# Performance work log

Hardware: AMD Instinct MI355X
Metric: run time of the kernel (lower is better)

## Reference

```python
import jax, jax.numpy as jnp
import numpy as np

H, D = 4, 32            # heads, per-head dim
HD = H * D              # hidden_dim = output_dim = 128
ND, NG = 10000, 30000   # num disease / gene nodes
E_DG, E_GD, E_GG = 150000, 150000, 300000
L = 2                   # num HGTConv layers


def setup_inputs() -> dict:
    key = jax.random.key(0)
    ks = jax.random.split(key, 16)
    s = 0.05
    return {
        "x_d": jax.random.normal(ks[0], (ND, HD), jnp.float32),
        "x_g": jax.random.normal(ks[1], (NG, HD), jnp.float32),
        "src_dg": jax.random.randint(ks[2], (E_DG,), 0, ND),
        "dst_dg": jax.random.randint(ks[3], (E_DG,), 0, NG),
        "src_gd": jax.random.randint(ks[4], (E_GD,), 0, NG),
        "dst_gd": jax.random.randint(ks[5], (E_GD,), 0, ND),
        "src_gg": jax.random.randint(ks[6], (E_GG,), 0, NG),
        "dst_gg": jax.random.randint(ks[7], (E_GG,), 0, NG),
        # fused K/Q/V projection per node type, stacked over layers
        "Wkqv_d": jax.random.normal(ks[8], (L, HD, 3 * HD), jnp.float32) * s,
        "bkqv_d": jnp.zeros((L, 3 * HD), jnp.float32),
        "Wkqv_g": jax.random.normal(ks[9], (L, HD, 3 * HD), jnp.float32) * s,
        "bkqv_g": jnp.zeros((L, 3 * HD), jnp.float32),
        # output linear per node type
        "Wout_d": jax.random.normal(ks[10], (L, HD, HD), jnp.float32) * s,
        "bout_d": jnp.zeros((L, HD), jnp.float32),
        "Wout_g": jax.random.normal(ks[11], (L, HD, HD), jnp.float32) * s,
        "bout_g": jnp.zeros((L, HD), jnp.float32),
        # learnable skip gates per node type
        "skip_d": jnp.ones((L,), jnp.float32),
        "skip_g": jnp.ones((L,), jnp.float32),
        # per edge-type relation matrices (key, message) and priors, 3 edge types
        "arel": jax.random.normal(ks[12], (L, 3, H, D, D), jnp.float32) * s,
        "mrel": jax.random.normal(ks[13], (L, 3, H, D, D), jnp.float32) * s,
        "prel": jnp.ones((L, 3, H), jnp.float32),
    }


def _hgt_forward(x_d, x_g, src_dg, dst_dg, src_gd, dst_gd, src_gg, dst_gg,
                 Wkqv_d, bkqv_d, Wkqv_g, bkqv_g, Wout_d, bout_d, Wout_g, bout_g,
                 skip_d, skip_g, arel, mrel, prel):
    scale = 1.0 / (D ** 0.5)
    for l in range(L):
        def kqv(x, W, b):
            t = (x @ W + b).reshape(-1, 3, H, D)
            return t[:, 0], t[:, 1], t[:, 2]

        k_d, q_d, v_d = kqv(x_d, Wkqv_d[l], bkqv_d[l])
        k_g, q_g, v_g = kqv(x_g, Wkqv_g[l], bkqv_g[l])

        def edge_msgs(k_src, v_src, q_dst, src, dst, et):
            # gather src K/V, transform by per-edge-type relation matrices
            ke = jnp.einsum('ehd,hdf->ehf', k_src[src], arel[l, et])  # [E,H,D]
            ve = jnp.einsum('ehd,hdf->ehf', v_src[src], mrel[l, et])  # [E,H,D]
            a = jnp.sum(q_dst[dst] * ke, axis=-1) * prel[l, et] * scale  # [E,H]
            return a, ve

        a_dg, v_dg = edge_msgs(k_d, v_d, q_g, src_dg, dst_dg, 0)
        a_gd, v_gd = edge_msgs(k_g, v_g, q_d, src_gd, dst_gd, 1)
        a_gg, v_gg = edge_msgs(k_g, v_g, q_g, src_gg, dst_gg, 2)

        def aggregate(alphas, vals, dsts, n):
            # segment softmax over ALL incoming edges of a dst node (across edge types)
            a = jnp.concatenate(alphas, axis=0)
            v = jnp.concatenate(vals, axis=0)
            d = jnp.concatenate(dsts, axis=0)
            amax = jax.ops.segment_max(a, d, num_segments=n)
            ex = jnp.exp(a - amax[d])
            den = jax.ops.segment_sum(ex, d, num_segments=n)
            w = ex / den[d]
            out = jax.ops.segment_sum(w[:, :, None] * v, d, num_segments=n)
            return out.reshape(n, HD)

        agg_g = aggregate([a_dg, a_gg], [v_dg, v_gg], [dst_dg, dst_gg], NG)
        agg_d = aggregate([a_gd], [v_gd], [dst_gd], ND)

        def update(agg, x, Wout, bout, skip):
            o = jax.nn.gelu(agg) @ Wout + bout
            g = jax.nn.sigmoid(skip)
            return g * o + (1.0 - g) * x

        x_d = update(agg_d, x_d, Wout_d[l], bout_d[l], skip_d[l])
        x_g = update(agg_g, x_g, Wout_g[l], bout_g[l], skip_g[l])
    return x_d, x_g


def reference(x_d, x_g, src_dg, dst_dg, src_gd, dst_gd, src_gg, dst_gg,
              Wkqv_d, bkqv_d, Wkqv_g, bkqv_g, Wout_d, bout_d, Wout_g, bout_g,
              skip_d, skip_g, arel, mrel, prel):
    return _hgt_forward(x_d, x_g, src_dg, dst_dg, src_gd, dst_gd, src_gg, dst_gg,
                        Wkqv_d, bkqv_d, Wkqv_g, bkqv_g, Wout_d, bout_d, Wout_g, bout_g,
                        skip_d, skip_g, arel, mrel, prel)
```

## Files before the change

### kernel.cpp

```cpp
#include <hip/hip_runtime.h>
#include <hip/hip_bf16.h>

#define H 4
#define D 32
#define HD 128
#define ND 10000
#define NG 30000
#define E_DG 150000
#define E_GD 150000
#define E_GG 300000
#define NE (E_DG + E_GD + E_GG)
#define EG (E_DG + E_GG)
#define NLAYER 2
#define NBG 30
#define NBD 10
#define OCG 640
#define OCD 384
#define GOFF ((size_t)ND * OCD)
#define NSCAT 2344
#define NGEMM0 1250
#define XLSTRIDE 136

typedef _Float16 f16;
typedef __attribute__((ext_vector_type(2))) _Float16 f16x2;
typedef __attribute__((ext_vector_type(8))) _Float16 f16x8;
typedef __attribute__((ext_vector_type(8))) unsigned short u16x8;
typedef __attribute__((ext_vector_type(4))) float f32x4;

__device__ __forceinline__ float bu(unsigned short u) {
    return __uint_as_float(((unsigned)u) << 16);
}
__device__ __forceinline__ float ldraw(const void* p, size_t i, bool isf32) {
    return isf32 ? ((const float*)p)[i] : bu(((const unsigned short*)p)[i]);
}
__device__ __forceinline__ float gelu(float v) {
    const float c = 0.79788456080286536f * (v + 0.044715f * v * v * v);
    return 0.5f * v * (1.0f + tanhf(c));
}

__device__ __forceinline__ void combine_one(
    int idx, int GENE, bool isf32,
    const void* W, const void* bvec,
    const void* arel, const void* mrel, const void* prel,
    f16* __restrict__ Wp, float* __restrict__ bp) {
    const int OC = GENE ? OCG : OCD;
    const int l = idx / (OC * 128);
    const int rem = idx - l * OC * 128;
    const int col = rem >> 7;
    const int d = rem & 127;
    const int g = col >> 7;
    const int jj = col & 127;
    const int h = jj >> 5, f = jj & 31;
    const size_t wbase = (size_t)l * 128 * 384;
    const size_t bbase = (size_t)l * 384;
    float val, bv = 0.f;
    if (g == 0) {
        val = ldraw(W, wbase + d * 384 + 128 + jj, isf32);
        bv = ldraw(bvec, bbase + 128 + jj, isf32);
    } else {
        const int et = GENE ? ((g <= 2) ? 1 : 2) : 0;
        const bool isk = (g & 1);
        const void* mat = isk ? arel : mrel;
        const size_t mbase = (((size_t)(l * 3 + et) * H + h) << 10) + f;
        const int sb = isk ? 0 : 256;
        val = 0.f;
        for (int dd = 0; dd < 32; dd++)
            val += ldraw(W, wbase + d * 384 + sb + h * 32 + dd, isf32) *
                   ldraw(mat, mbase + dd * 32, isf32);
        if (d == 0)
            for (int dd = 0; dd < 32; dd++)
                bv += ldraw(bvec, bbase + sb + h * 32 + dd, isf32) *
                      ldraw(mat, mbase + dd * 32, isf32);
        if (isk) {
            const float sc = ldraw(prel, (size_t)(l * 3 + et) * H + h, isf32) *
                             (0.17677669529663689f * 1.4426950408889634f);
            val *= sc;
            bv *= sc;
        }
    }
    Wp[(size_t)l * 4 * OC * 32 + ((size_t)(d >> 5) * OC + col) * 32 + (d & 31)] = (f16)val;
    if (d == 0) bp[l * OC + col] = bv;
}

__global__ __launch_bounds__(256) void k_prep0(
    const void* x0,
    const void* wkqvd_r, const void* bkqvd_r,
    const void* wkqvg_r, const void* bkqvg_r,
    const void* arel_r, const void* mrel_r, const void* prel_r,
    const void* woutd_r, const void* woutg_r,
    const void* boutd_r, const void* boutg_r,
    const void* skipd_r, const void* skipg_r,
    f16* __restrict__ Wp_d, float* __restrict__ bp_d,
    f16* __restrict__ Wp_g, float* __restrict__ bp_g,
    f16* __restrict__ Wpod, f16* __restrict__ Wpog,
    float* __restrict__ boutc_d, float* __restrict__ boutc_g,
    float* __restrict__ gates, int* __restrict__ flag,
    int* __restrict__ cnt, int* __restrict__ ready) {
    const int tid = threadIdx.x;
    __shared__ int sbad;
    if (tid == 0) sbad = 0;
    __syncthreads();
    {
        const unsigned short* xs = (const unsigned short*)x0;
        int bad = 0;
        for (int i = tid; i < 1024; i += 256)
            if (!(fabsf(bu(xs[i])) < 1e6f)) bad = 1;
        if (bad) sbad = 1;
    }
    __syncthreads();
    const bool isf32 = (sbad != 0);

    const int b = blockIdx.x;
    if (b < 1280) {
        int idx = b * 256 + tid;
        const int nd = NLAYER * OCD * 128;
        const int ng = NLAYER * OCG * 128;
        const int np = 2 * NLAYER * 128 * 128;
        if (idx < nd) {
            combine_one(idx, 0, isf32, wkqvd_r, bkqvd_r, arel_r, mrel_r, prel_r, Wp_d, bp_d);
        } else if ((idx -= nd) < ng) {
            combine_one(idx, 1, isf32, wkqvg_r, bkqvg_r, arel_r, mrel_r, prel_r, Wp_g, bp_g);
        } else if ((idx -= ng) < np) {
            const int type = idx >= NLAYER * 128 * 128;
            int rem = idx - type * NLAYER * 128 * 128;
            const int l = rem / (128 * 128);
            rem -= l * 128 * 128;
            const int d = rem >> 7, col = rem & 127;
            const float w = ldraw(type ? woutg_r : woutd_r,
                                  (size_t)l * 128 * 128 + d * 128 + col, isf32);
            f16* out = (type ? Wpog : Wpod) +
                ((size_t)l * 4 + (d >> 5)) * 128 * 32 + col * 32 + (d & 31);
            *out = (f16)w;
        }
    } else if (b == 1280) {
        if (tid < NBG + NBD) ready[tid] = 0;
        if (tid == 0) {
            flag[0] = isf32 ? 1 : 0;
            gates[0] = 1.f / (1.f + expf(-ldraw(skipd_r, 0, isf32)));
            gates[1] = 1.f / (1.f + expf(-ldraw(skipg_r, 0, isf32)));
            gates[2] = 1.f / (1.f + expf(-ldraw(skipd_r, 1, isf32)));
            gates[3] = 1.f / (1.f + expf(-ldraw(skipg_r, 1, isf32)));
        }
        for (int i = tid; i < NLAYER * 128; i += 256) {
            boutc_d[i] = ldraw(boutd_r, i, isf32);
            boutc_g[i] = ldraw(boutg_r, i, isf32);
        }
    } else {
        const int base = (b - 1281) * 1000;
        for (int i = tid; i < 1000; i += 256) cnt[base + i] = 0;
    }
}

__global__ __launch_bounds__(256) void k_hist(
    const int* __restrict__ dst_dg, const int* __restrict__ dst_gg,
    const int* __restrict__ dst_gd,
    int* __restrict__ cnt_g, int* __restrict__ cnt_d) {
    const int i = blockIdx.x * 256 + threadIdx.x;
    if (i < E_DG) atomicAdd(cnt_g + dst_dg[i], 1);
    else if (i < EG) atomicAdd(cnt_g + dst_gg[i - E_DG], 1);
    else if (i < NE) atomicAdd(cnt_d + dst_gd[i - EG], 1);
}

__global__ __launch_bounds__(256) void k_scan(
    const int* __restrict__ cnt_g, const int* __restrict__ cnt_d,
    int* __restrict__ ready,
    int* __restrict__ rp_g, int* __restrict__ cur_g,
    int* __restrict__ rp_d, int* __restrict__ cur_d) {
    const int b = blockIdx.x;
    const int tid = threadIdx.x;
    const bool isg = (b < NBG);
    const int* cnt = isg ? cnt_g : cnt_d;
    int* rp = isg ? rp_g : rp_d;
    int* cur = isg ? cur_g : cur_d;
    const int n = isg ? NG : ND;
    const int lb = isg ? b : (b - NBG);
    const int i0 = lb * 1024 + tid * 4;
    int v[4];
    int t = 0;
#pragma unroll
    for (int j = 0; j < 4; j++) {
        v[j] = (i0 + j < n) ? cnt[i0 + j] : 0;
        t += v[j];
    }
    __shared__ int sdata[256];
    __shared__ int red2[256];
    __shared__ int s_off;
    sdata[tid] = t;
    __syncthreads();
    for (int d = 1; d < 256; d <<= 1) {
        const int u = (tid >= d) ? sdata[tid - d] : 0;
        __syncthreads();
        sdata[tid] += u;
        __syncthreads();
    }
    const int total = sdata[255];
    if (tid == 0) atomicExch(&ready[b], total + 1);
    const int p0 = isg ? 0 : NBG;
    const int npred = b - p0;
    int part = 0;
    for (int i = tid; i < npred; i += 256) {
        int vv;
        do { vv = atomicAdd(&ready[p0 + i], 0); } while (vv == 0);
        part += vv - 1;
    }
    red2[tid] = part;
    __syncthreads();
    for (int d = 128; d > 0; d >>= 1) {
        if (tid < d) red2[tid] += red2[tid + d];
        __syncthreads();
    }
    if (tid == 0) s_off = red2[0];
    __syncthreads();
    int run = s_off + sdata[tid] - t;
#pragma unroll
    for (int j = 0; j < 4; j++) {
        if (i0 + j < n) {
            cur[i0 + j] = run;
            run += v[j];
            rp[i0 + j + 1] = run;
        }
    }
    if (tid == 0 && lb == 0) rp[0] = 0;
}

__global__ __launch_bounds__(256) void k_scatter_gemm0(
    const int* __restrict__ src_dg, const int* __restrict__ dst_dg,
    const int* __restrict__ src_gg, const int* __restrict__ dst_gg,
    const int* __restrict__ src_gd, const int* __restrict__ dst_gd,
    int* __restrict__ cur_g, int* __restrict__ cur_d,
    int* __restrict__ edges_g, int* __restrict__ edges_d,
    const void* xd_r, const void* xg_r, const int* __restrict__ flag,
    const f16* __restrict__ Wpd, const float* __restrict__ bpd,
    const f16* __restrict__ Wpg, const float* __restrict__ bpg,
    f16* __restrict__ tab) {
    __shared__ f16 xls[32 * XLSTRIDE];
    if (blockIdx.x < NSCAT) {
        const int i = blockIdx.x * 256 + threadIdx.x;
        if (i < E_DG) {
            const int pos = atomicAdd(cur_g + dst_dg[i], 1);
            edges_g[pos] = src_dg[i] * OCD + 128;
        } else if (i < EG) {
            const int j = i - E_DG;
            const int pos = atomicAdd(cur_g + dst_gg[j], 1);
            edges_g[pos] = (int)GOFF + src_gg[j] * OCG + 384;
        } else if (i < NE) {
            const int j = i - EG;
            const int pos = atomicAdd(cur_d + dst_gd[j], 1);
            edges_d[pos] = (int)GOFF + src_gd[j] * OCG + 128;
        }
        return;
    }
    const bool isf32 = (*flag != 0);
    const int tid = threadIdx.x;
    const int mt0 = (blockIdx.x - NSCAT) * 2;
    for (int i = tid; i < 1024; i += 256) {
        const int row = i >> 5;
        const int c4 = (i & 31) * 4;
        const int gnode = mt0 * 16 + row;
        const bool gene = (gnode >= ND);
        const void* xr = gene ? xg_r : xd_r;
        const size_t base = (size_t)(gene ? gnode - ND : gnode) * 128 + c4;
        float4 v;
        if (isf32) {
            v = *(const float4*)((const float*)xr + base);
        } else {
            const ushort4 u = *(const ushort4*)((const unsigned short*)xr + base);
            v = make_float4(bu(u.x), bu(u.y), bu(u.z), bu(u.w));
        }
        f16* dst = xls + row * XLSTRIDE + c4;
        dst[0] = (f16)v.x; dst[1] = (f16)v.y; dst[2] = (f16)v.z; dst[3] = (f16)v.w;
    }
    __syncthreads();

    const int wv = tid >> 6, lane = tid & 63;
    const int r = lane & 15, q4 = lane >> 4;
    const int n0 = (mt0 * 16 >= ND) ? 10 : 6;
    const int n1 = ((mt0 + 1) * 16 >= ND) ? 10 : 6;
    for (int it = wv; it < n0 + n1; it += 4) {
        const int mtl = (it < n0) ? 0 : 1;
        const int ntl = (it < n0) ? it : (it - n0);
        const int node0 = (mt0 + mtl) * 16;
        const bool gene = (node0 >= ND);
        const int OC = gene ? OCG : OCD;
        const f16* Wp = gene ? Wpg : Wpd;
        const float* bias = gene ? bpg : bpd;
        f16* out = gene ? (tab + GOFF) : tab;
        const int trow0 = node0 - (gene ? ND : 0);
        const int col0 = ntl << 6;
        f32x4 acc0 = {0.f, 0.f, 0.f, 0.f};
        f32x4 acc1 = acc0, acc2 = acc0, acc3 = acc0;
#pragma unroll
        for (int kb = 0; kb < 4; kb++) {
            const f16x8 a = *(const f16x8*)(xls + (mtl * 16 + r) * XLSTRIDE + kb * 32 + q4 * 8);
            const f16* wb = Wp + ((size_t)kb * OC + col0 + r) * 32 + q4 * 8;
            const f16x8 b0 = *(const f16x8*)(wb);
            const f16x8 b1 = *(const f16x8*)(wb + 512);
            const f16x8 b2 = *(const f16x8*)(wb + 1024);
            const f16x8 b3 = *(const f16x8*)(wb + 1536);
            acc0 = __builtin_amdgcn_mfma_f32_16x16x32_f16(a, b0, acc0, 0, 0, 0);
            acc1 = __builtin_amdgcn_mfma_f32_16x16x32_f16(a, b1, acc1, 0, 0, 0);
            acc2 = __builtin_amdgcn_mfma_f32_16x16x32_f16(a, b2, acc2, 0, 0, 0);
            acc3 = __builtin_amdgcn_mfma_f32_16x16x32_f16(a, b3, acc3, 0, 0, 0);
        }
        const f32x4 accs[4] = {acc0, acc1, acc2, acc3};
#pragma unroll
        for (int t = 0; t < 4; t++) {
            const int col = col0 + t * 16 + r;
            const float bb = bias[col];
#pragma unroll
            for (int reg = 0; reg < 4; reg++)
                out[(size_t)(trow0 + q4 * 4 + reg) * OC + col] = (f16)(accs[t][reg] + bb);
        }
    }
}

__global__ __launch_bounds__(256) void k_agg(
    const int* __restrict__ rp_g, const int* __restrict__ edges_g,
    const int* __restrict__ rp_d, const int* __restrict__ edges_d,
    const f16* __restrict__ tab, f16* __restrict__ gagg) {
    const int wid = blockIdx.x * 4 + (threadIdx.x >> 6);
    const int lane = threadIdx.x & 63;
    const int slot = lane >> 4, sub = lane & 15;

    int node, row;
    const int *rp, *edges;
    size_t qoff;
    if (wid < NG) {
        node = wid; rp = rp_g; edges = edges_g;
        qoff = GOFF + (size_t)node * OCG;
        row = ND + node;
    } else {
        node = wid - NG; rp = rp_d; edges = edges_d;
        qoff = (size_t)node * OCD;
        row = node;
    }

    union U { f16x8 v; f16x2 p[4]; };
    U q;
    q.v = *(const f16x8*)(tab + qoff + sub * 8);

    float s = 0.f;
    float acc[8];
#pragma unroll
    for (int i = 0; i < 8; i++) acc[i] = 0.f;

    const int r0 = rp[node], r1 = rp[node + 1];
    int e = r0 + slot;

    auto kvload = [&](int rec, U& k, U& v) {
        const f16* p = tab + (size_t)rec + sub * 8;
        k.v = *(const f16x8*)p;
        v.v = *(const f16x8*)(p + 128);
    };

    int recA0 = (e < r1) ? edges[e] : 0;
    int recB0 = (e + 4 < r1) ? edges[e + 4] : 0;
    U kA0, vA0, kB0, vB0;
    kvload(recA0, kA0, vA0);
    kvload(recB0, kB0, vB0);
    int recA1 = (e + 8 < r1) ? edges[e + 8] : 0;
    int recB1 = (e + 12 < r1) ? edges[e + 12] : 0;

    while (e < r1) {
        const int recA2 = (e + 16 < r1) ? edges[e + 16] : 0;
        const int recB2 = (e + 20 < r1) ? edges[e + 20] : 0;
        U kA1, vA1, kB1, vB1;
        kvload(recA1, kA1, vA1);
        kvload(recB1, kB1, vB1);

        float pA = __builtin_amdgcn_fdot2(q.p[0], kA0.p[0], 0.f, false);
        float pB = __builtin_amdgcn_fdot2(q.p[0], kB0.p[0], 0.f, false);
        pA = __builtin_amdgcn_fdot2(q.p[1], kA0.p[1], pA, false);
        pB = __builtin_amdgcn_fdot2(q.p[1], kB0.p[1], pB, false);
        pA = __builtin_amdgcn_fdot2(q.p[2], kA0.p[2], pA, false);
        pB = __builtin_amdgcn_fdot2(q.p[2], kB0.p[2], pB, false);
        pA = __builtin_amdgcn_fdot2(q.p[3], kA0.p[3], pA, false);
        pB = __builtin_amdgcn_fdot2(q.p[3], kB0.p[3], pB, false);
        pA += __shfl_xor(pA, 1);
        pB += __shfl_xor(pB, 1);
        pA += __shfl_xor(pA, 2);
        pB += __shfl_xor(pB, 2);
        const float eaA = exp2f(pA);
        const float eaB = (e + 4 < r1) ? exp2f(pB) : 0.f;
        s += eaA + eaB;
#pragma unroll
        for (int i = 0; i < 8; i++)
            acc[i] = fmaf(eaB, (float)vB0.v[i], fmaf(eaA, (float)vA0.v[i], acc[i]));
        recA0 = recA1; recB0 = recB1; recA1 = recA2; recB1 = recB2;
        kA0 = kA1; vA0 = vA1; kB0 = kB1; vB0 = vB1;
        e += 8;
    }

#pragma unroll
    for (int mask = 16; mask <= 32; mask <<= 1) {
        s += __shfl_xor(s, mask);
#pragma unroll
        for (int i = 0; i < 8; i++) acc[i] += __shfl_xor(acc[i], mask);
    }

    const float inv = (s > 0.f) ? (1.f / s) : 0.f;
    if (slot == 0) {
        f16x8 o;
#pragma unroll
        for (int i = 0; i < 8; i++) o[i] = (f16)gelu(acc[i] * inv);
        *(f16x8*)(gagg + (size_t)row * HD + sub * 8) = o;
    }
}

__global__ __launch_bounds__(256) void k_updgemm(
    const f16* __restrict__ gagg,
    const f16* __restrict__ Wpod0, const f16* __restrict__ Wpog0,
    const float* __restrict__ boutc_d0, const float* __restrict__ boutc_g0,
    const float* __restrict__ gates,
    const void* xd_r, const void* xg_r, const int* __restrict__ flag,
    f16* __restrict__ xball,
    const f16* __restrict__ Wpd1, const float* __restrict__ bpd1,
    const f16* __restrict__ Wpg1, const float* __restrict__ bpg1,
    f16* __restrict__ tab) {
    __shared__ f16 xls[32 * XLSTRIDE];
    const bool isf32 = (*flag != 0);
    const int tid = threadIdx.x;
    const int wv = tid >> 6, lane = tid & 63;
    const int r = lane & 15, q4 = lane >> 4;

    {
        const int mtl = wv >> 1, nt = wv & 1;
        const int mtile = blockIdx.x * 2 + mtl;
        const int node0 = mtile * 16;
        const bool gene = (node0 >= ND);
        const f16* Wp = gene ? Wpog0 : Wpod0;
        const float* bias = gene ? boutc_g0 : boutc_d0;
        const float g = gates[gene ? 1 : 0];
        const int col0 = nt << 6;
        f32x4 acc0 = {0.f, 0.f, 0.f, 0.f};
        f32x4 acc1 = acc0, acc2 = acc0, acc3 = acc0;
#pragma unroll
        for (int kb = 0; kb < 4; kb++) {
            const f16x8 a = *(const f16x8*)(gagg + (size_t)(node0 + r) * 128 + kb * 32 + q4 * 8);
            const f16* wb = Wp + ((size_t)kb * 128 + col0 + r) * 32 + q4 * 8;
            const f16x8 b0 = *(const f16x8*)(wb);
            const f16x8 b1 = *(const f16x8*)(wb + 512);
            const f16x8 b2 = *(const f16x8*)(wb + 1024);
            const f16x8 b3 = *(const f16x8*)(wb + 1536);
            acc0 = __builtin_amdgcn_mfma_f32_16x16x32_f16(a, b0, acc0, 0, 0, 0);
            acc1 = __builtin_amdgcn_mfma_f32_16x16x32_f16(a, b1, acc1, 0, 0, 0);
            acc2 = __builtin_amdgcn_mfma_f32_16x16x32_f16(a, b2, acc2, 0, 0, 0);
            acc3 = __builtin_amdgcn_mfma_f32_16x16x32_f16(a, b3, acc3, 0, 0, 0);
        }
        const f32x4 accs[4] = {acc0, acc1, acc2, acc3};
        const void* xr = gene ? xg_r : xd_r;
        const int lrow0 = node0 - (gene ? ND : 0);
#pragma unroll
        for (int t = 0; t < 4; t++) {
            const int col = col0 + t * 16 + r;
            const float bb = bias[col];
#pragma unroll
            for (int reg = 0; reg < 4; reg++) {
                const int rr = q4 * 4 + reg;
                const float xo = ldraw(xr, (size_t)(lrow0 + rr) * 128 + col, isf32);
                const float xn = g * (accs[t][reg] + bb) + (1.f - g) * xo;
                xls[(mtl * 16 + rr) * XLSTRIDE + col] = (f16)xn;
                xball[(size_t)(node0 + rr) * 128 + col] = (f16)xn;
            }
        }
    }
    __syncthreads();

    const int mt0 = blockIdx.x * 2;
    const int n0 = ((mt0 * 16) >= ND) ? 10 : 6;
    const int n1 = (((mt0 + 1) * 16) >= ND) ? 10 : 6;
    for (int it = wv; it < n0 + n1; it += 4) {
        const int mtl = (it < n0) ? 0 : 1;
        const int ntl = (it < n0) ? it : (it - n0);
        const int node0 = (mt0 + mtl) * 16;
        const bool gene = (node0 >= ND);
        const int OC = gene ? OCG : OCD;
        const f16* Wp = gene ? Wpg1 : Wpd1;
        const float* bias = gene ? bpg1 : bpd1;
        f16* out = gene ? (tab + GOFF) : tab;
        const int trow0 = node0 - (gene ? ND : 0);
        const int col0 = ntl << 6;
        f32x4 acc0 = {0.f, 0.f, 0.f, 0.f};
        f32x4 acc1 = acc0, acc2 = acc0, acc3 = acc0;
#pragma unroll
        for (int kb = 0; kb < 4; kb++) {
            const f16x8 a = *(const f16x8*)(xls + (mtl * 16 + r) * XLSTRIDE + kb * 32 + q4 * 8);
            const f16* wb = Wp + ((size_t)kb * OC + col0 + r) * 32 + q4 * 8;
            const f16x8 b0 = *(const f16x8*)(wb);
            const f16x8 b1 = *(const f16x8*)(wb + 512);
            const f16x8 b2 = *(const f16x8*)(wb + 1024);
            const f16x8 b3 = *(const f16x8*)(wb + 1536);
            acc0 = __builtin_amdgcn_mfma_f32_16x16x32_f16(a, b0, acc0, 0, 0, 0);
            acc1 = __builtin_amdgcn_mfma_f32_16x16x32_f16(a, b1, acc1, 0, 0, 0);
            acc2 = __builtin_amdgcn_mfma_f32_16x16x32_f16(a, b2, acc2, 0, 0, 0);
            acc3 = __builtin_amdgcn_mfma_f32_16x16x32_f16(a, b3, acc3, 0, 0, 0);
        }
        const f32x4 accs[4] = {acc0, acc1, acc2, acc3};
#pragma unroll
        for (int t = 0; t < 4; t++) {
            const int col = col0 + t * 16 + r;
            const float bb = bias[col];
#pragma unroll
            for (int reg = 0; reg < 4; reg++)
                out[(size_t)(trow0 + q4 * 4 + reg) * OC + col] = (f16)(accs[t][reg] + bb);
        }
    }
}

__global__ __launch_bounds__(256) void k_upd1(
    const f16* __restrict__ gagg,
    const f16* __restrict__ Wpod1, const f16* __restrict__ Wpog1,
    const float* __restrict__ boutc_d1, const float* __restrict__ boutc_g1,
    const float* __restrict__ gates,
    const f16* __restrict__ xball, float* __restrict__ dout) {
    const int w = blockIdx.x * 4 + (threadIdx.x >> 6);
    const int nt = w / 2500, mt = w - nt * 2500;
    const int node0 = mt << 4;
    const bool gene = (node0 >= ND);
    const f16* Wp = gene ? Wpog1 : Wpod1;
    const float* bias = gene ? boutc_g1 : boutc_d1;
    const float g = gates[gene ? 1 : 0];
    const int lane = threadIdx.x & 63;
    const int r = lane & 15, q4 = lane >> 4;
    const int col0 = nt << 6;
    f32x4 acc0 = {0.f, 0.f, 0.f, 0.f};
    f32x4 acc1 = acc0, acc2 = acc0, acc3 = acc0;
#pragma unroll
    for (int kb = 0; kb < 4; kb++) {
        const f16x8 a = *(const f16x8*)(gagg + (size_t)(node0 + r) * 128 + kb * 32 + q4 * 8);
        const f16* wb = Wp + ((size_t)kb * 128 + col0 + r) * 32 + q4 * 8;
        const f16x8 b0 = *(const f16x8*)(wb);
        const f16x8 b1 = *(const f16x8*)(wb + 512);
        const f16x8 b2 = *(const f16x8*)(wb + 1024);
        const f16x8 b3 = *(const f16x8*)(wb + 1536);
        acc0 = __builtin_amdgcn_mfma_f32_16x16x32_f16(a, b0, acc0, 0, 0, 0);
        acc1 = __builtin_amdgcn_mfma_f32_16x16x32_f16(a, b1, acc1, 0, 0, 0);
        acc2 = __builtin_amdgcn_mfma_f32_16x16x32_f16(a, b2, acc2, 0, 0, 0);
        acc3 = __builtin_amdgcn_mfma_f32_16x16x32_f16(a, b3, acc3, 0, 0, 0);
    }
    const f32x4 accs[4] = {acc0, acc1, acc2, acc3};
#pragma unroll
    for (int t = 0; t < 4; t++) {
        const int col = col0 + t * 16 + r;
        const float bb = bias[col];
#pragma unroll
        for (int reg = 0; reg < 4; reg++) {
            const size_t idx = (size_t)(node0 + q4 * 4 + reg) * 128 + col;
            dout[idx] = g * (accs[t][reg] + bb) + (1.f - g) * (float)xball[idx];
        }
    }
}

static inline size_t alignup(size_t v) { return (v + 15) & ~(size_t)15; }

extern "C" void kernel_launch(void* const* d_in, const int* in_sizes, int n_in,
                              void* d_out, int out_size, void* d_ws, size_t ws_size,
                              hipStream_t stream) {
    (void)in_sizes; (void)n_in; (void)out_size; (void)ws_size;
    const int* src_dg = (const int*)d_in[2];
    const int* dst_dg = (const int*)d_in[3];
    const int* src_gd = (const int*)d_in[4];
    const int* dst_gd = (const int*)d_in[5];
    const int* src_gg = (const int*)d_in[6];
    const int* dst_gg = (const int*)d_in[7];

    float* ws = (float*)d_ws;
    int* flag = (int*)ws; ws += 16;
    int* cnt_g  = (int*)ws; ws += alignup(NG);
    int* cnt_d  = (int*)ws; ws += alignup(ND);
    int* rp_g   = (int*)ws; ws += alignup(NG + 1);
    int* rp_d   = (int*)ws; ws += alignup(ND + 1);
    int* cur_g  = (int*)ws; ws += alignup(NG);
    int* cur_d  = (int*)ws; ws += alignup(ND);
    int* ready  = (int*)ws; ws += 64;
    int* edges_g = (int*)ws; ws += alignup(EG);
    int* edges_d = (int*)ws; ws += alignup(E_GD);
    float* bp_d = ws; ws += alignup((size_t)NLAYER * OCD);
    float* bp_g = ws; ws += alignup((size_t)NLAYER * OCG);
    float* boutc_d = ws; ws += alignup((size_t)NLAYER * 128);
    float* boutc_g = ws; ws += alignup((size_t)NLAYER * 128);
    float* gates = ws; ws += 16;
    f16* Wp_d = (f16*)ws; ws += alignup((size_t)NLAYER * 4 * OCD * 32 / 2);
    f16* Wp_g = (f16*)ws; ws += alignup((size_t)NLAYER * 4 * OCG * 32 / 2);
    f16* Wpod = (f16*)ws; ws += alignup((size_t)NLAYER * 4 * 128 * 32 / 2);
    f16* Wpog = (f16*)ws; ws += alignup((size_t)NLAYER * 4 * 128 * 32 / 2);
    f16* xball = (f16*)ws; ws += alignup((size_t)(ND + NG) * HD / 2);
    f16* gagg  = (f16*)ws; ws += alignup((size_t)(ND + NG) * HD / 2);
    f16* tab   = (f16*)ws; ws += alignup(((size_t)ND * OCD + (size_t)NG * OCG) / 2);

    k_prep0<<<1321, 256, 0, stream>>>(
        d_in[0],
        d_in[8], d_in[9], d_in[10], d_in[11],
        d_in[18], d_in[19], d_in[20],
        d_in[12], d_in[14], d_in[13], d_in[15], d_in[16], d_in[17],
        Wp_d, bp_d, Wp_g, bp_g, Wpod, Wpog, boutc_d, boutc_g,
        gates, flag, cnt_g, ready);
    k_hist<<<NSCAT, 256, 0, stream>>>(dst_dg, dst_gg, dst_gd, cnt_g, cnt_d);
    k_scan<<<NBG + NBD, 256, 0, stream>>>(cnt_g, cnt_d, ready, rp_g, cur_g, rp_d, cur_d);
    k_scatter_gemm0<<<NSCAT + NGEMM0, 256, 0, stream>>>(
        src_dg, dst_dg, src_gg, dst_gg, src_gd, dst_gd,
        cur_g, cur_d, edges_g, edges_d,
        d_in[0], d_in[1], flag,
        Wp_d, bp_d, Wp_g, bp_g, tab);
    k_agg<<<(NG + ND) / 4, 256, 0, stream>>>(rp_g, edges_g, rp_d, edges_d, tab, gagg);
    k_updgemm<<<(ND + NG) / 32, 256, 0, stream>>>(
        gagg, Wpod, Wpog, boutc_d, boutc_g, gates,
        d_in[0], d_in[1], flag, xball,
        Wp_d + (size_t)4 * OCD * 32, bp_d + OCD,
        Wp_g + (size_t)4 * OCG * 32, bp_g + OCG, tab);
    k_agg<<<(NG + ND) / 4, 256, 0, stream>>>(rp_g, edges_g, rp_d, edges_d, tab, gagg);
    k_upd1<<<(ND + NG) / 32, 256, 0, stream>>>(
        gagg, Wpod + (size_t)4 * 128 * 32, Wpog + (size_t)4 * 128 * 32,
        boutc_d + 128, boutc_g + 128, gates + 2, xball, (float*)d_out);
}
```

Measured before the change: 363.0 us.

## Record per-edge rank in histogram pass and fold histogram into prep kernel

The edge histogram now runs as extra blocks of the prep kernel and stores the atomicAdd return value as a per-edge rank. The scatter pass then places each edge at rp[dst] + rank, so the second round of atomics on a cursor array is gone and one kernel launch is removed. Counters are zeroed with a memset instead of dedicated blocks. The cost is an extra rank array of NE ints that is written in one pass and read back in the next.

```diff
diff --git a/kernel.cpp b/kernel.cpp
--- a/kernel.cpp
+++ b/kernel.cpp
@@ -95,8 +95,19 @@
     f16* __restrict__ Wpod, f16* __restrict__ Wpog,
     float* __restrict__ boutc_d, float* __restrict__ boutc_g,
     float* __restrict__ gates, int* __restrict__ flag,
-    int* __restrict__ cnt, int* __restrict__ ready) {
+    const int* __restrict__ dst_dg, const int* __restrict__ dst_gg,
+    const int* __restrict__ dst_gd,
+    int* __restrict__ cnt_g, int* __restrict__ cnt_d,
+    int* __restrict__ rank, int* __restrict__ ready) {
     const int tid = threadIdx.x;
+    const int b = blockIdx.x;
+    if (b >= 1281) {
+        const int i = (b - 1281) * 256 + tid;
+        if (i < E_DG) rank[i] = atomicAdd(cnt_g + dst_dg[i], 1);
+        else if (i < EG) rank[i] = atomicAdd(cnt_g + dst_gg[i - E_DG], 1);
+        else if (i < NE) rank[i] = atomicAdd(cnt_d + dst_gd[i - EG], 1);
+        return;
+    }
     __shared__ int sbad;
     if (tid == 0) sbad = 0;
     __syncthreads();
@@ -110,7 +121,6 @@
     __syncthreads();
     const bool isf32 = (sbad != 0);
 
-    const int b = blockIdx.x;
     if (b < 1280) {
         int idx = b * 256 + tid;
         const int nd = NLAYER * OCD * 128;
@@ -132,7 +142,7 @@
                 ((size_t)l * 4 + (d >> 5)) * 128 * 32 + col * 32 + (d & 31);
             *out = (f16)w;
         }
-    } else if (b == 1280) {
+    } else {
         if (tid < NBG + NBD) ready[tid] = 0;
         if (tid == 0) {
             flag[0] = isf32 ? 1 : 0;
@@ -145,33 +155,18 @@
             boutc_d[i] = ldraw(boutd_r, i, isf32);
             boutc_g[i] = ldraw(boutg_r, i, isf32);
         }
-    } else {
-        const int base = (b - 1281) * 1000;
-        for (int i = tid; i < 1000; i += 256) cnt[base + i] = 0;
-    }
-}
-
-__global__ __launch_bounds__(256) void k_hist(
-    const int* __restrict__ dst_dg, const int* __restrict__ dst_gg,
-    const int* __restrict__ dst_gd,
-    int* __restrict__ cnt_g, int* __restrict__ cnt_d) {
-    const int i = blockIdx.x * 256 + threadIdx.x;
-    if (i < E_DG) atomicAdd(cnt_g + dst_dg[i], 1);
-    else if (i < EG) atomicAdd(cnt_g + dst_gg[i - E_DG], 1);
-    else if (i < NE) atomicAdd(cnt_d + dst_gd[i - EG], 1);
+    }
 }
 
 __global__ __launch_bounds__(256) void k_scan(
     const int* __restrict__ cnt_g, const int* __restrict__ cnt_d,
     int* __restrict__ ready,
-    int* __restrict__ rp_g, int* __restrict__ cur_g,
-    int* __restrict__ rp_d, int* __restrict__ cur_d) {
+    int* __restrict__ rp_g, int* __restrict__ rp_d) {
     const int b = blockIdx.x;
     const int tid = threadIdx.x;
     const bool isg = (b < NBG);
     const int* cnt = isg ? cnt_g : cnt_d;
     int* rp = isg ? rp_g : rp_d;
-    int* cur = isg ? cur_g : cur_d;
     const int n = isg ? NG : ND;
     const int lb = isg ? b : (b - NBG);
     const int i0 = lb * 1024 + tid * 4;
@@ -215,7 +210,6 @@
 #pragma unroll
     for (int j = 0; j < 4; j++) {
         if (i0 + j < n) {
-            cur[i0 + j] = run;
             run += v[j];
             rp[i0 + j + 1] = run;
         }
@@ -227,7 +221,8 @@
     const int* __restrict__ src_dg, const int* __restrict__ dst_dg,
     const int* __restrict__ src_gg, const int* __restrict__ dst_gg,
     const int* __restrict__ src_gd, const int* __restrict__ dst_gd,
-    int* __restrict__ cur_g, int* __restrict__ cur_d,
+    const int* __restrict__ rp_g, const int* __restrict__ rp_d,
+    const int* __restrict__ rank,
     int* __restrict__ edges_g, int* __restrict__ edges_d,
     const void* xd_r, const void* xg_r, const int* __restrict__ flag,
     const f16* __restrict__ Wpd, const float* __restrict__ bpd,
@@ -237,16 +232,13 @@
     if (blockIdx.x < NSCAT) {
         const int i = blockIdx.x * 256 + threadIdx.x;
         if (i < E_DG) {
-            const int pos = atomicAdd(cur_g + dst_dg[i], 1);
-            edges_g[pos] = src_dg[i] * OCD + 128;
+            edges_g[rp_g[dst_dg[i]] + rank[i]] = src_dg[i] * OCD + 128;
         } else if (i < EG) {
             const int j = i - E_DG;
-            const int pos = atomicAdd(cur_g + dst_gg[j], 1);
-            edges_g[pos] = (int)GOFF + src_gg[j] * OCG + 384;
+            edges_g[rp_g[dst_gg[j]] + rank[i]] = (int)GOFF + src_gg[j] * OCG + 384;
         } else if (i < NE) {
             const int j = i - EG;
-            const int pos = atomicAdd(cur_d + dst_gd[j], 1);
-            edges_d[pos] = (int)GOFF + src_gd[j] * OCG + 128;
+            edges_d[rp_d[dst_gd[j]] + rank[i]] = (int)GOFF + src_gd[j] * OCG + 128;
         }
         return;
     }
@@ -570,8 +562,7 @@
     int* cnt_d  = (int*)ws; ws += alignup(ND);
     int* rp_g   = (int*)ws; ws += alignup(NG + 1);
     int* rp_d   = (int*)ws; ws += alignup(ND + 1);
-    int* cur_g  = (int*)ws; ws += alignup(NG);
-    int* cur_d  = (int*)ws; ws += alignup(ND);
+    int* rank   = (int*)ws; ws += alignup(NE);
     int* ready  = (int*)ws; ws += 64;
     int* edges_g = (int*)ws; ws += alignup(EG);
     int* edges_d = (int*)ws; ws += alignup(E_GD);
@@ -588,18 +579,19 @@
     f16* gagg  = (f16*)ws; ws += alignup((size_t)(ND + NG) * HD / 2);
     f16* tab   = (f16*)ws; ws += alignup(((size_t)ND * OCD + (size_t)NG * OCG) / 2);
 
-    k_prep0<<<1321, 256, 0, stream>>>(
+    hipMemsetAsync(cnt_g, 0, (size_t)(NG + ND) * sizeof(int), stream);
+    k_prep0<<<1281 + NSCAT, 256, 0, stream>>>(
         d_in[0],
         d_in[8], d_in[9], d_in[10], d_in[11],
         d_in[18], d_in[19], d_in[20],
         d_in[12], d_in[14], d_in[13], d_in[15], d_in[16], d_in[17],
         Wp_d, bp_d, Wp_g, bp_g, Wpod, Wpog, boutc_d, boutc_g,
-        gates, flag, cnt_g, ready);
-    k_hist<<<NSCAT, 256, 0, stream>>>(dst_dg, dst_gg, dst_gd, cnt_g, cnt_d);
-    k_scan<<<NBG + NBD, 256, 0, stream>>>(cnt_g, cnt_d, ready, rp_g, cur_g, rp_d, cur_d);
+        gates, flag,
+        dst_dg, dst_gg, dst_gd, cnt_g, cnt_d, rank, ready);
+    k_scan<<<NBG + NBD, 256, 0, stream>>>(cnt_g, cnt_d, ready, rp_g, rp_d);
     k_scatter_gemm0<<<NSCAT + NGEMM0, 256, 0, stream>>>(
         src_dg, dst_dg, src_gg, dst_gg, src_gd, dst_gd,
-        cur_g, cur_d, edges_g, edges_d,
+        rp_g, rp_d, rank, edges_g, edges_d,
         d_in[0], d_in[1], flag,
         Wp_d, bp_d, Wp_g, bp_g, tab);
     k_agg<<<(NG + ND) / 4, 256, 0, stream>>>(rp_g, edges_g, rp_d, edges_d, tab, gagg);
```

Measured after the change: 328.3 us. 1.11x faster.
